# Performance work log

Hardware: AMD Instinct MI355X
Metric: run time of the kernel (lower is better)

The kernel has to match this reference:

```python
import jax, jax.numpy as jnp
import numpy as np


def _reflect(x, size):
    # PyTorch grid_sample reflection padding, align_corners=False:
    # reflect about borders at -0.5 and size-0.5, then clip to [0, size-1].
    x = x + 0.5
    x = jnp.mod(x, 2.0 * size)
    x = jnp.where(x >= size, 2.0 * size - x, x)
    x = x - 0.5
    return jnp.clip(x, 0.0, size - 1.0)


def _grid_sample_one(img, grid):
    # img: (H, W, C); grid: (H, W, 2) with (x, y) in [-1, 1]
    H, W, _ = img.shape
    # unnormalize, align_corners=False
    ix = ((grid[..., 0] + 1.0) * W - 1.0) * 0.5
    iy = ((grid[..., 1] + 1.0) * H - 1.0) * 0.5
    ix = _reflect(ix, W)
    iy = _reflect(iy, H)
    x0 = jnp.floor(ix)
    y0 = jnp.floor(iy)
    wx = (ix - x0)[..., None]
    wy = (iy - y0)[..., None]
    x0i = jnp.clip(x0, 0, W - 1).astype(jnp.int32)
    x1i = jnp.clip(x0 + 1.0, 0, W - 1).astype(jnp.int32)
    y0i = jnp.clip(y0, 0, H - 1).astype(jnp.int32)
    y1i = jnp.clip(y0 + 1.0, 0, H - 1).astype(jnp.int32)
    Ia = img[y0i, x0i]  # (H, W, C)
    Ib = img[y0i, x1i]
    Ic = img[y1i, x0i]
    Id = img[y1i, x1i]
    return (Ia * (1 - wx) * (1 - wy) + Ib * wx * (1 - wy)
            + Ic * (1 - wx) * wy + Id * wx * wy)


def _displace(image, displacement_map, amplitude, angle):
    N, H, W, C = image.shape
    # base sampling grid, torch.linspace(-1, 1, size) endpoints included
    gy, gx = jnp.meshgrid(jnp.linspace(-1.0, 1.0, H, dtype=image.dtype),
                          jnp.linspace(-1.0, 1.0, W, dtype=image.dtype),
                          indexing='ij')
    base = jnp.stack([gx, gy], axis=-1)  # (H, W, 2) as (x, y)
    # bilinear resize (half-pixel centers == torch align_corners=False)
    dm = jax.image.resize(displacement_map,
                          (N, H, W, displacement_map.shape[-1]),
                          method='bilinear')
    if dm.shape[-1] == 3:
        dm = jnp.mean(dm, axis=-1)  # (N, H, W)
    else:
        dm = dm[..., 0]
    d = dm * amplitude[:, None, None]
    dx = jnp.cos(angle)[:, None, None] * d / (W - 1) * 2.0
    dy = jnp.sin(angle)[:, None, None] * d / (H - 1) * 2.0
    grid = base[None] + jnp.stack([dx, dy], axis=-1)  # (N, H, W, 2)
    return jax.vmap(_grid_sample_one)(image, grid)  # (N, H, W, C)


def setup_inputs() -> dict:
    key = jax.random.key(0)
    k1, k2, k3, k4 = jax.random.split(key, 4)
    N, H, W, C = 8, 1024, 1024, 3
    image = jax.random.normal(k1, (N, H, W, C), dtype=jnp.float32)
    displacement_map = jax.random.uniform(k2, (N, 512, 512, 3), dtype=jnp.float32)
    amplitude = jax.random.uniform(k3, (N,), dtype=jnp.float32) * 20.0  # pixels
    angle = jax.random.uniform(k4, (N,), dtype=jnp.float32) * 2.0 * np.pi
    return {"image": image, "displacement_map": displacement_map,
            "amplitude": amplitude, "angle": angle}


def reference(image, displacement_map, amplitude, angle):
    return _displace(image, displacement_map, amplitude, angle)
```

## Files before the change

kernel.cpp:

```cpp
#include <hip/hip_runtime.h>
#include <math.h>

__global__ __launch_bounds__(256) void prep_kernel(
    const float* __restrict__ dmap, const float* __restrict__ amp,
    const float* __restrict__ ang, float* __restrict__ sc,
    float* __restrict__ rd, long long npix, int N, float fx, float fy) {
    long long p = (long long)blockIdx.x * 256 + threadIdx.x;
    if (p < npix) {
        const float* s = dmap + p * 3;
        rd[p] = s[0] + s[1] + s[2];
    }
    if (blockIdx.x == 0 && (int)threadIdx.x < N) {
        int i = threadIdx.x;
        float s_, c_;
        sincosf(ang[i], &s_, &c_);
        float a = amp[i] * (1.0f / 3.0f);
        sc[2 * i]     = c_ * a * fx;
        sc[2 * i + 1] = s_ * a * fy;
    }
}

__global__ __launch_bounds__(256) void displace_main(
    const float* __restrict__ img,
    const float* __restrict__ rd,
    const float* __restrict__ sc,
    float* __restrict__ out)
{
    const int lin  = (int)blockIdx.x;
    const int n    = lin & 7;
    const int rest = lin >> 3;
    const int h0   = (rest >> 2) << 2;
    const int w    = ((rest & 3) << 8) + (int)threadIdx.x;

    const float scx = sc[2 * n];
    const float scy = sc[2 * n + 1];
    const float* ibase = img + (long long)n * (1024 * 1024 * 3);
    const float* rbase = rd + n * (512 * 512);

    const int dx0 = max((w - 1) >> 1, 0);
    const int dx1 = min((w + 1) >> 1, 511);
    const float tx = (w & 1) ? 0.25f : 0.75f;
    const float C = 1024.0f / 1023.0f;
    const float uxb = (float)w * C;

    #pragma unroll
    for (int k = 0; k < 4; ++k) {
        const int h = h0 + k;
        const int dy0 = max((h - 1) >> 1, 0);
        const int dy1 = min((h + 1) >> 1, 511);
        const float ty = (h & 1) ? 0.25f : 0.75f;
        const float* r0 = rbase + (dy0 << 9);
        const float* r1 = rbase + (dy1 << 9);

        float a0 = r0[dx0], b0 = r0[dx1];
        float a1 = r1[dx0], b1 = r1[dx1];
        float m0 = fmaf(b0 - a0, tx, a0);
        float m1 = fmaf(b1 - a1, tx, a1);
        float ds = fmaf(m1 - m0, ty, m0);

        float ux = fmaf(ds, scx, uxb);
        float uy = fmaf(ds, scy, (float)h * C);

        ux = fabsf(ux); if (ux >= 1024.0f) ux = 2048.0f - ux;
        uy = fabsf(uy); if (uy >= 1024.0f) uy = 2048.0f - uy;
        float ix = fminf(fmaxf(ux - 0.5f, 0.0f), 1023.0f);
        float iy = fminf(fmaxf(uy - 0.5f, 0.0f), 1023.0f);

        int ix0 = (int)ix;
        int iy0 = (int)iy;
        float wx = ix - (float)ix0;
        float wy = iy - (float)iy0;
        int ix1 = min(ix0 + 1, 1023);
        int iy1 = min(iy0 + 1, 1023);

        const float* Ia = ibase + ((iy0 << 10) + ix0) * 3;
        const float* Ib = ibase + ((iy0 << 10) + ix1) * 3;
        const float* Ic = ibase + ((iy1 << 10) + ix0) * 3;
        const float* Id = ibase + ((iy1 << 10) + ix1) * 3;

        const float wa = (1.0f - wx) * (1.0f - wy);
        const float wb = wx * (1.0f - wy);
        const float wc = (1.0f - wx) * wy;
        const float wd = wx * wy;

        float* o = out + (((long long)(n << 10 | h) << 10) + w) * 3;
        o[0] = Ia[0] * wa + Ib[0] * wb + Ic[0] * wc + Id[0] * wd;
        o[1] = Ia[1] * wa + Ib[1] * wb + Ic[1] * wc + Id[1] * wd;
        o[2] = Ia[2] * wa + Ib[2] * wb + Ic[2] * wc + Id[2] * wd;
    }
}

__device__ __forceinline__ float reflect_dyn(float x, float size) {
    x += 0.5f;
    float two = 2.0f * size;
    x = x - floorf(x / two) * two;
    if (x >= size) x = two - x;
    x -= 0.5f;
    return fminf(fmaxf(x, 0.0f), size - 1.0f);
}

__global__ __launch_bounds__(256) void displace_fallback(
    const float* __restrict__ img, const float* __restrict__ dmap,
    const float* __restrict__ amp, const float* __restrict__ ang,
    float* __restrict__ out, int N, int H, int W, int DH, int DW)
{
    long long idx = (long long)blockIdx.x * blockDim.x + threadIdx.x;
    long long total = (long long)N * H * W;
    if (idx >= total) return;
    int w = (int)(idx % W);
    long long t = idx / W;
    int h = (int)(t % H);
    int n = (int)(t / H);

    float sx = (w + 0.5f) * ((float)DW / (float)W) - 0.5f;
    float sy = (h + 0.5f) * ((float)DH / (float)H) - 0.5f;
    float fx = floorf(sx), fy = floorf(sy);
    float tx = sx - fx, ty = sy - fy;
    int dx0 = max(0, min(DW - 1, (int)fx));
    int dx1 = max(0, min(DW - 1, (int)fx + 1));
    int dy0 = max(0, min(DH - 1, (int)fy));
    int dy1 = max(0, min(DH - 1, (int)fy + 1));
    const float* dbase = dmap + (long long)n * DH * DW * 3;
    const float* p00 = dbase + ((long long)dy0 * DW + dx0) * 3;
    const float* p01 = dbase + ((long long)dy0 * DW + dx1) * 3;
    const float* p10 = dbase + ((long long)dy1 * DW + dx0) * 3;
    const float* p11 = dbase + ((long long)dy1 * DW + dx1) * 3;
    float m00 = p00[0] + p00[1] + p00[2];
    float m01 = p01[0] + p01[1] + p01[2];
    float m10 = p10[0] + p10[1] + p10[2];
    float m11 = p11[0] + p11[1] + p11[2];
    float dmv = ((m00 * (1.0f - tx) + m01 * tx) * (1.0f - ty)
               + (m10 * (1.0f - tx) + m11 * tx) * ty) * (1.0f / 3.0f);
    float a = amp[n], an = ang[n], sa, ca;
    sincosf(an, &sa, &ca);
    float d = dmv * a;
    float gx = -1.0f + 2.0f * (float)w / (float)(W - 1) + ca * d * (2.0f / (float)(W - 1));
    float gy = -1.0f + 2.0f * (float)h / (float)(H - 1) + sa * d * (2.0f / (float)(H - 1));
    float ixf2 = ((gx + 1.0f) * (float)W - 1.0f) * 0.5f;
    float iyf2 = ((gy + 1.0f) * (float)H - 1.0f) * 0.5f;
    ixf2 = reflect_dyn(ixf2, (float)W);
    iyf2 = reflect_dyn(iyf2, (float)H);
    float x0f = floorf(ixf2), y0f = floorf(iyf2);
    float wx = ixf2 - x0f, wy = iyf2 - y0f;
    int ix0 = min((int)x0f, W - 1);
    int ix1 = min((int)x0f + 1, W - 1);
    int iy0 = min((int)y0f, H - 1);
    int iy1 = min((int)y0f + 1, H - 1);
    const float* ibase = img + (long long)n * H * W * 3;
    const float* Ia = ibase + ((long long)iy0 * W + ix0) * 3;
    const float* Ib = ibase + ((long long)iy0 * W + ix1) * 3;
    const float* Ic = ibase + ((long long)iy1 * W + ix0) * 3;
    const float* Id = ibase + ((long long)iy1 * W + ix1) * 3;
    float wa = (1.0f - wx) * (1.0f - wy);
    float wb = wx * (1.0f - wy);
    float wc = (1.0f - wx) * wy;
    float wd = wx * wy;
    float* o = out + idx * 3;
    #pragma unroll
    for (int c = 0; c < 3; ++c)
        o[c] = Ia[c] * wa + Ib[c] * wb + Ic[c] * wc + Id[c] * wd;
}

extern "C" void kernel_launch(void* const* d_in, const int* in_sizes, int n_in,
                              void* d_out, int out_size, void* d_ws, size_t ws_size,
                              hipStream_t stream) {
    const float* img  = (const float*)d_in[0];
    const float* dmap = (const float*)d_in[1];
    const float* amp  = (const float*)d_in[2];
    const float* ang  = (const float*)d_in[3];
    float* out = (float*)d_out;

    int N = in_sizes[2];
    long long hw  = (long long)in_sizes[0] / ((long long)N * 3);
    int H = (int)llround(sqrt((double)hw));
    int W = H;
    long long dhw = (long long)in_sizes[1] / ((long long)N * 3);
    int DH = (int)llround(sqrt((double)dhw));
    int DW = DH;

    size_t need = 256 + (size_t)N * DH * DW * sizeof(float);

    if (H == 1024 && W == 1024 && DH == 512 && DW == 512 && N == 8 &&
        ws_size >= need) {
        float* sc = (float*)d_ws;
        float* rd = (float*)((char*)d_ws + 256);

        long long npix = (long long)N * DH * DW;
        int pgrid = (int)((npix + 255) / 256);
        prep_kernel<<<pgrid, 256, 0, stream>>>(
            dmap, amp, ang, sc, rd, npix, N,
            (float)W / (float)(W - 1), (float)H / (float)(H - 1));

        displace_main<<<8192, 256, 0, stream>>>(img, rd, sc, out);
    } else {
        long long total = (long long)N * H * W;
        int block = 256;
        long long grid = (total + block - 1) / block;
        displace_fallback<<<(dim3)(unsigned)grid, block, 0, stream>>>(
            img, dmap, amp, ang, out, N, H, W, DH, DW);
    }
}
```

Before: 232.3 us.

## Stage displacement tile in LDS and vectorize gather taps and output stores

Each block now loads its 4x130 patch of the reduced displacement map into shared memory once, instead of every thread issuing four scattered global loads per row. Image taps are fetched as one unaligned 4-float vector load per corner, shifted back by one float at the very last pixel so it never reads past the buffer. Output pixels are written as a single 3-float vector store. The intent is fewer memory instructions per pixel, at the cost of a barrier, some redundant loads and unaligned vector accesses.

New measurement: 233.8 us. Within noise of the previous version (+0.6%).

```diff
diff --git a/kernel.cpp b/kernel.cpp
--- a/kernel.cpp
+++ b/kernel.cpp
@@ -1,5 +1,10 @@
 #include <hip/hip_runtime.h>
 #include <math.h>
+
+typedef float vf4 __attribute__((ext_vector_type(4)));
+typedef vf4 uvf4 __attribute__((aligned(4)));
+typedef float vf3 __attribute__((ext_vector_type(3)));
+typedef vf3 uvf3 __attribute__((aligned(4)));
 
 __global__ __launch_bounds__(256) void prep_kernel(
     const float* __restrict__ dmap, const float* __restrict__ amp,
@@ -18,6 +23,15 @@
         sc[2 * i]     = c_ * a * fx;
         sc[2 * i + 1] = s_ * a * fy;
     }
+}
+
+__device__ __forceinline__ void tap_load(const float* p, const float* plast,
+                                         float& r, float& g, float& b) {
+    int off = (p == plast) ? 1 : 0;
+    uvf4 v = *(const uvf4*)(p - off);
+    r = off ? v.y : v.x;
+    g = off ? v.z : v.y;
+    b = off ? v.w : v.z;
 }
 
 __global__ __launch_bounds__(256) void displace_main(
@@ -30,15 +44,30 @@
     const int n    = lin & 7;
     const int rest = lin >> 3;
     const int h0   = (rest >> 2) << 2;
-    const int w    = ((rest & 3) << 8) + (int)threadIdx.x;
+    const int w0   = (rest & 3) << 8;
+    const int w    = w0 + (int)threadIdx.x;
+
+    const float* rbase = rd + (n << 18);
+    const int base_x = (w0 >> 1) - 1;
+    const int base_y = (h0 >> 1) - 1;
+
+    __shared__ float lds[4][132];
+    for (int e = (int)threadIdx.x; e < 520; e += 256) {
+        int j = e / 130;
+        int i = e - j * 130;
+        int row = min(max(base_y + j, 0), 511);
+        int col = min(max(base_x + i, 0), 511);
+        lds[j][i] = rbase[(row << 9) + col];
+    }
+    __syncthreads();
 
     const float scx = sc[2 * n];
     const float scy = sc[2 * n + 1];
     const float* ibase = img + (long long)n * (1024 * 1024 * 3);
-    const float* rbase = rd + n * (512 * 512);
-
-    const int dx0 = max((w - 1) >> 1, 0);
-    const int dx1 = min((w + 1) >> 1, 511);
+    const float* plast = img + (8LL * 1024 * 1024 * 3 - 3);
+
+    const int sx0 = ((w - 1) >> 1) - base_x;
+    const int sx1 = ((w + 1) >> 1) - base_x;
     const float tx = (w & 1) ? 0.25f : 0.75f;
     const float C = 1024.0f / 1023.0f;
     const float uxb = (float)w * C;
@@ -46,14 +75,12 @@
     #pragma unroll
     for (int k = 0; k < 4; ++k) {
         const int h = h0 + k;
-        const int dy0 = max((h - 1) >> 1, 0);
-        const int dy1 = min((h + 1) >> 1, 511);
+        const int sy0 = ((h - 1) >> 1) - base_y;
+        const int sy1 = ((h + 1) >> 1) - base_y;
         const float ty = (h & 1) ? 0.25f : 0.75f;
-        const float* r0 = rbase + (dy0 << 9);
-        const float* r1 = rbase + (dy1 << 9);
-
-        float a0 = r0[dx0], b0 = r0[dx1];
-        float a1 = r1[dx0], b1 = r1[dx1];
+
+        float a0 = lds[sy0][sx0], b0 = lds[sy0][sx1];
+        float a1 = lds[sy1][sx0], b1 = lds[sy1][sx1];
         float m0 = fmaf(b0 - a0, tx, a0);
         float m1 = fmaf(b1 - a1, tx, a1);
         float ds = fmaf(m1 - m0, ty, m0);
@@ -73,20 +100,27 @@
         int ix1 = min(ix0 + 1, 1023);
         int iy1 = min(iy0 + 1, 1023);
 
-        const float* Ia = ibase + ((iy0 << 10) + ix0) * 3;
-        const float* Ib = ibase + ((iy0 << 10) + ix1) * 3;
-        const float* Ic = ibase + ((iy1 << 10) + ix0) * 3;
-        const float* Id = ibase + ((iy1 << 10) + ix1) * 3;
+        const float* Pa = ibase + ((iy0 << 10) + ix0) * 3;
+        const float* Pb = ibase + ((iy0 << 10) + ix1) * 3;
+        const float* Pc = ibase + ((iy1 << 10) + ix0) * 3;
+        const float* Pd = ibase + ((iy1 << 10) + ix1) * 3;
+
+        float ar, ag, ab, br, bg, bb, cr, cg, cb, dr, dg, db;
+        tap_load(Pa, plast, ar, ag, ab);
+        tap_load(Pb, plast, br, bg, bb);
+        tap_load(Pc, plast, cr, cg, cb);
+        tap_load(Pd, plast, dr, dg, db);
 
         const float wa = (1.0f - wx) * (1.0f - wy);
         const float wb = wx * (1.0f - wy);
         const float wc = (1.0f - wx) * wy;
         const float wd = wx * wy;
 
-        float* o = out + (((long long)(n << 10 | h) << 10) + w) * 3;
-        o[0] = Ia[0] * wa + Ib[0] * wb + Ic[0] * wc + Id[0] * wd;
-        o[1] = Ia[1] * wa + Ib[1] * wb + Ic[1] * wc + Id[1] * wd;
-        o[2] = Ia[2] * wa + Ib[2] * wb + Ic[2] * wc + Id[2] * wd;
+        uvf3 o;
+        o.x = ar * wa + br * wb + cr * wc + dr * wd;
+        o.y = ag * wa + bg * wb + cg * wc + dg * wd;
+        o.z = ab * wa + bb * wb + cb * wc + db * wd;
+        *(uvf3*)(out + (long long)(((n << 10 | h) << 10) + w) * 3) = o;
     }
 }
 
```
